# Performance work log

Hardware: AMD Instinct MI355X
Metric: run time of the kernel (lower is better)

Reference implementation:

```python
import jax, jax.numpy as jnp
import numpy as np

NUM_HEADS = 16
LAMBDA = 0.1
HADAMARD_SCALE = 0.05
ROPE_BASE = 10000.0


def _rope(t):
    # t: [B, H, S, hd] -- rotary embedding (half-split convention)
    hd = t.shape[-1]
    S = t.shape[2]
    half = hd // 2
    inv_freq = 1.0 / (ROPE_BASE ** (jnp.arange(half, dtype=jnp.float32) / half))
    ang = jnp.arange(S, dtype=jnp.float32)[:, None] * inv_freq[None, :]  # [S, half]
    cos = jnp.cos(ang).astype(t.dtype)
    sin = jnp.sin(ang).astype(t.dtype)
    t1, t2 = t[..., :half], t[..., half:]
    return jnp.concatenate([t1 * cos - t2 * sin, t2 * cos + t1 * sin], axis=-1)


def _rotate_half(t):
    half = t.shape[-1] // 2
    return jnp.concatenate([-t[..., half:], t[..., :half]], axis=-1)


def setup_inputs() -> dict:
    key = jax.random.key(0)
    ks = jax.random.split(key, 6)
    B, S, D = 2, 2048, 1024
    scale = 1.0 / np.sqrt(D).astype(np.float32)
    x = jax.random.normal(ks[0], (B, S, D), jnp.float32)
    Wq = jax.random.normal(ks[1], (D, D), jnp.float32) * scale
    Wk = jax.random.normal(ks[2], (D, D), jnp.float32) * scale
    Wv = jax.random.normal(ks[3], (D, D), jnp.float32) * scale
    Wo = jax.random.normal(ks[4], (D, D), jnp.float32) * scale
    gate_w = jax.random.normal(ks[5], (D // NUM_HEADS,), jnp.float32) * 0.01
    return {"x": x, "Wq": Wq, "Wk": Wk, "Wv": Wv, "Wo": Wo, "gate_w": gate_w}


def reference(x, Wq, Wk, Wv, Wo, gate_w):
    B, S, D = x.shape
    H = NUM_HEADS
    hd = D // H

    def heads(W):
        return (x @ W.T).reshape(B, S, H, hd).transpose(0, 2, 1, 3)  # [B,H,S,hd]

    Q = _rope(heads(Wq))
    K = _rope(heads(Wk))
    V = heads(Wv)

    causal = jnp.tril(jnp.ones((S, S), dtype=bool))
    inv_sqrt_d = 1.0 / jnp.sqrt(jnp.asarray(hd, x.dtype))

    def attend(q, k):
        # first-order + lambda * second-order (elementwise-squared) scores
        s = (jnp.einsum('bhsd,bhtd->bhst', q, k)
             + LAMBDA * jnp.einsum('bhsd,bhtd->bhst', q * q, k * k)) * inv_sqrt_d
        s = jnp.where(causal, s, jnp.asarray(-1e9, s.dtype))
        a = jax.nn.softmax(s, axis=-1)
        return jnp.einsum('bhst,bhtd->bhsd', a, V)

    out1 = attend(Q, K)                                  # standard pass
    out2 = attend(_rotate_half(Q), _rotate_half(K))      # rotated second pass

    # hadamard gate mix of the two passes
    out = 0.5 * (out1 + out2) + HADAMARD_SCALE * (out1 * out2) * gate_w

    out = out.transpose(0, 2, 1, 3).reshape(B, S, D)
    return out @ Wo.T
```

## Files before the change

### kernel.cpp

```cpp
#include <hip/hip_runtime.h>

typedef unsigned short u16;
typedef __attribute__((ext_vector_type(4))) unsigned short u16x4;
typedef __attribute__((ext_vector_type(8))) unsigned short u16x8;
typedef __attribute__((ext_vector_type(8))) short s16x8;
typedef __attribute__((ext_vector_type(4))) float f32x4;

__device__ __forceinline__ u16 f2bf(float f) {
  unsigned int u = __float_as_uint(f);
  u += 0x7FFFu + ((u >> 16) & 1u);
  return (u16)(u >> 16);
}
__device__ __forceinline__ float bf2f(u16 h) {
  return __uint_as_float(((unsigned int)h) << 16);
}

__device__ __forceinline__ void gload_lds16(const u16* g, u16* l) {
  __builtin_amdgcn_global_load_lds(
      (const __attribute__((address_space(1))) unsigned int*)(g),
      (__attribute__((address_space(3))) unsigned int*)(l), 16, 0, 0);
}

__global__ __launch_bounds__(256) void cvt_kernel(const float* __restrict__ src,
                                                  u16* __restrict__ dst, int n4) {
  int i = blockIdx.x * 256 + threadIdx.x;
  if (i >= n4) return;
  float4 v = reinterpret_cast<const float4*>(src)[i];
  u16x4 o;
  o.x = f2bf(v.x); o.y = f2bf(v.y); o.z = f2bf(v.z); o.w = f2bf(v.w);
  reinterpret_cast<u16x4*>(dst)[i] = o;
}

__global__ __launch_bounds__(256) void cvt_w(const float* __restrict__ Wq,
                                             const float* __restrict__ Wk,
                                             const float* __restrict__ Wv,
                                             const float* __restrict__ Wo,
                                             u16* __restrict__ wbf, u16* __restrict__ wobf) {
  int blk = blockIdx.x;
  int sel = blk >> 10;
  const float* src = (sel == 0) ? Wq : (sel == 1) ? Wk : (sel == 2) ? Wv : Wo;
  u16* dst = (sel < 3) ? (wbf + (size_t)sel * 1048576) : wobf;
  int i = (blk & 1023) * 256 + threadIdx.x;
  float4 v = reinterpret_cast<const float4*>(src)[i];
  u16x4 o;
  o.x = f2bf(v.x); o.y = f2bf(v.y); o.z = f2bf(v.z); o.w = f2bf(v.w);
  reinterpret_cast<u16x4*>(dst)[i] = o;
}

__device__ __forceinline__ void store_out(float* p, float v) { *p = v; }
__device__ __forceinline__ void store_out(u16* p, float v) { *p = f2bf(v); }

template <typename OutT, int WM, int WN>
__global__ __launch_bounds__(256) void gemm_bt(const u16* __restrict__ A,
                                               const u16* __restrict__ Bw,
                                               OutT* __restrict__ C, int N, int K) {
  __shared__ u16 As[WM * 2048];
  __shared__ u16 Bs[WN * 2048];
  const int tid = threadIdx.x;
  const int lane = tid & 63;
  const int wave = tid >> 6;
  const int wm = wave >> 1, wn = wave & 1;
  const int lh = lane & 15, quad = lane >> 4;
  const int q8 = quad * 8;
  const int m0 = blockIdx.y * (WM * 32), n0 = blockIdx.x * (WN * 32);
  constexpr int NCH = 4 * (WM + WN);
  constexpr int PER = NCH / 4;

  f32x4 acc[WM][WN];
#pragma unroll
  for (int i = 0; i < WM; ++i)
#pragma unroll
    for (int j = 0; j < WN; ++j) { acc[i][j][0] = 0.f; acc[i][j][1] = 0.f; acc[i][j][2] = 0.f; acc[i][j][3] = 0.f; }

  const int nkt = K >> 6;
  for (int kt = 0; kt < nkt; ++kt) {
    const int kb = kt * 64;
    __syncthreads();
#pragma unroll
    for (int i = 0; i < PER; ++i) {
      const int c = wave * PER + i;
      if (c < 4 * WM) {
        const int rb = c >> 1, kk2 = c & 1;
        gload_lds16(A + (size_t)(m0 + rb * 16 + lh) * K + kb + kk2 * 32 + q8,
                    &As[c * 512 + lane * 8]);
      } else {
        const int cb = c - 4 * WM;
        const int rb = cb >> 1, kk2 = cb & 1;
        gload_lds16(Bw + (size_t)(n0 + rb * 16 + lh) * K + kb + kk2 * 32 + q8,
                    &Bs[cb * 512 + lane * 8]);
      }
    }
    __syncthreads();
#pragma unroll
    for (int kk2 = 0; kk2 < 2; ++kk2) {
      s16x8 af[WM], bf4[WN];
#pragma unroll
      for (int mb = 0; mb < WM; ++mb)
        af[mb] = *reinterpret_cast<const s16x8*>(&As[((wm * WM + mb) * 2 + kk2) * 512 + lane * 8]);
#pragma unroll
      for (int nb = 0; nb < WN; ++nb)
        bf4[nb] = *reinterpret_cast<const s16x8*>(&Bs[((wn * WN + nb) * 2 + kk2) * 512 + lane * 8]);
#pragma unroll
      for (int mb = 0; mb < WM; ++mb)
#pragma unroll
        for (int nb = 0; nb < WN; ++nb)
          acc[mb][nb] = __builtin_amdgcn_mfma_f32_16x16x32_bf16(af[mb], bf4[nb], acc[mb][nb], 0, 0, 0);
    }
  }
#pragma unroll
  for (int mb = 0; mb < WM; ++mb)
#pragma unroll
    for (int nb = 0; nb < WN; ++nb) {
      const int col = n0 + wn * (WN * 16) + nb * 16 + lh;
#pragma unroll
      for (int r = 0; r < 4; ++r) {
        const int row = m0 + wm * (WM * 16) + mb * 16 + quad * 4 + r;
        store_out(&C[(size_t)row * N + col], acc[mb][nb][r]);
      }
    }
}

__global__ __launch_bounds__(256) void qkv_gemm(const u16* __restrict__ A,
                                                const u16* __restrict__ Bw,
                                                u16* __restrict__ raw,
                                                u16* __restrict__ Qs,
                                                u16* __restrict__ Kb,
                                                u16* __restrict__ K2b) {
  __shared__ u16 As[8192];
  __shared__ u16 Bs[8192];
  const int tid = threadIdx.x;
  const int lane = tid & 63;
  const int wave = tid >> 6;
  const int wm = wave >> 1, wn = wave & 1;
  const int lh = lane & 15, quad = lane >> 4;
  const int q8 = quad * 8;
  const int bx = blockIdx.x;
  const int m0 = blockIdx.y * 128, n0 = bx * 128;
  const int K = 1024;

  f32x4 acc[4][4];
#pragma unroll
  for (int i = 0; i < 4; ++i)
#pragma unroll
    for (int j = 0; j < 4; ++j) { acc[i][j][0] = 0.f; acc[i][j][1] = 0.f; acc[i][j][2] = 0.f; acc[i][j][3] = 0.f; }

  for (int kt = 0; kt < 16; ++kt) {
    const int kb = kt * 64;
    __syncthreads();
#pragma unroll
    for (int i = 0; i < 8; ++i) {
      const int c = wave * 8 + i;
      if (c < 16) {
        const int rb = c >> 1, kk2 = c & 1;
        gload_lds16(A + (size_t)(m0 + rb * 16 + lh) * K + kb + kk2 * 32 + q8,
                    &As[c * 512 + lane * 8]);
      } else {
        const int cb = c - 16;
        const int rb = cb >> 1, kk2 = cb & 1;
        gload_lds16(Bw + (size_t)(n0 + rb * 16 + lh) * K + kb + kk2 * 32 + q8,
                    &Bs[cb * 512 + lane * 8]);
      }
    }
    __syncthreads();
#pragma unroll
    for (int kk2 = 0; kk2 < 2; ++kk2) {
      s16x8 af[4], bf4[4];
#pragma unroll
      for (int mb = 0; mb < 4; ++mb)
        af[mb] = *reinterpret_cast<const s16x8*>(&As[((wm * 4 + mb) * 2 + kk2) * 512 + lane * 8]);
#pragma unroll
      for (int nb = 0; nb < 4; ++nb)
        bf4[nb] = *reinterpret_cast<const s16x8*>(&Bs[((wn * 4 + nb) * 2 + kk2) * 512 + lane * 8]);
#pragma unroll
      for (int mb = 0; mb < 4; ++mb)
#pragma unroll
        for (int nb = 0; nb < 4; ++nb)
          acc[mb][nb] = __builtin_amdgcn_mfma_f32_16x16x32_bf16(af[mb], bf4[nb], acc[mb][nb], 0, 0, 0);
    }
  }

  if (bx < 16) {
    const bool isQ = (bx < 8);
#pragma unroll
    for (int nb = 0; nb < 2; ++nb) {
      const int d = nb * 16 + lh;
      const float invf = __expf((float)d * -0.2878231366f);
      const int col = n0 + wn * 64 + nb * 16 + lh;
      const int ch = col & 1023;
      const int h = ch >> 6;
#pragma unroll
      for (int mb = 0; mb < 4; ++mb)
#pragma unroll
        for (int r = 0; r < 4; ++r) {
          const int row = m0 + wm * 64 + mb * 16 + quad * 4 + r;
          const int s = row & 2047, b = row >> 11;
          float ang = (float)s * invf;
          float sv, cv;
          __sincosf(ang, &sv, &cv);
          const float v1 = acc[mb][nb][r], v2 = acc[mb][nb + 2][r];
          const float e0 = v1 * cv - v2 * sv;
          const float e1 = v2 * cv + v1 * sv;
          const size_t ofs = (size_t)((b * 16 + h) * 2048 + s) * 64 + d;
          if (isQ) {
            Qs[ofs]      = f2bf(e0 * 0.125f);
            Qs[ofs + 32] = f2bf(e1 * 0.125f);
          } else {
            Kb[ofs]       = f2bf(e0);
            Kb[ofs + 32]  = f2bf(e1);
            K2b[ofs]      = f2bf(e0 * e0);
            K2b[ofs + 32] = f2bf(e1 * e1);
          }
        }
    }
  } else {
#pragma unroll
    for (int mb = 0; mb < 4; ++mb)
#pragma unroll
      for (int nb = 0; nb < 4; ++nb) {
        const int col = n0 + wn * 64 + nb * 16 + lh;
#pragma unroll
        for (int r = 0; r < 4; ++r) {
          const int row = m0 + wm * 64 + mb * 16 + quad * 4 + r;
          raw[(size_t)row * 3072 + col] = f2bf(acc[mb][nb][r]);
        }
      }
  }
}

__global__ __launch_bounds__(256) void transpose_v(const u16* __restrict__ raw,
                                                   u16* __restrict__ Vt) {
  int st = blockIdx.x, bh = blockIdx.y;
  int b = bh >> 4, h = bh & 15;
  __shared__ u16 tile[64 * 72];
  int tid = threadIdx.x;
#pragma unroll
  for (int it = 0; it < 4; ++it) {
    int c = it * 256 + tid;
    int sr = c >> 4, d4 = c & 15;
    u16x4 v = *reinterpret_cast<const u16x4*>(
        raw + (size_t)(b * 2048 + st * 64 + sr) * 3072 + 2048 + h * 64 + d4 * 4);
    *reinterpret_cast<u16x4*>(&tile[sr * 72 + d4 * 4]) = v;
  }
  __syncthreads();
#pragma unroll
  for (int it = 0; it < 4; ++it) {
    int c = it * 256 + tid;
    int dd = c >> 4, s4 = c & 15;
    u16x4 v;
#pragma unroll
    for (int j = 0; j < 4; ++j) v[j] = tile[(s4 * 4 + j) * 72 + dd];
    *reinterpret_cast<u16x4*>(Vt + (size_t)(bh * 64 + dd) * 2048 + st * 64 + s4 * 4) = v;
  }
}

__global__ __launch_bounds__(256, 2) void attn_kernel(const u16* __restrict__ Qs,
                                                      const u16* __restrict__ Kb,
                                                      const u16* __restrict__ K2b,
                                                      const u16* __restrict__ Vt,
                                                      const float* __restrict__ gate,
                                                      u16* __restrict__ attn,
                                                      float* __restrict__ Opart,
                                                      float* __restrict__ Lpart,
                                                      float* __restrict__ Opart2,
                                                      float* __restrict__ Lpart2) {
  const int bx = blockIdx.x;
  int qi, kt0, kt1, half, which;
  bool split;
  if (bx < 16) {
    qi = 15 - (bx >> 1); half = bx & 1; split = true; which = 0;
    const int nk = qi + 1; kt0 = half * nk; kt1 = kt0 + nk - 1;
  } else if (bx < 24) {
    const int t = bx - 16;
    qi = 7 - (t >> 1); half = t & 1; split = true; which = 1;
    const int nk = qi + 1; kt0 = half * nk; kt1 = kt0 + nk - 1;
  } else {
    qi = 27 - bx; split = false; which = 0; half = 0; kt0 = 0; kt1 = 2 * qi + 1;
  }
  const int bh = blockIdx.y;
  const int tid = threadIdx.x, lane = tid & 63, wave = tid >> 6;
  const int lh = lane & 15, quad = lane >> 4;
  const int b = bh >> 4, h = bh & 15;
  __shared__ u16 stageS[2][8192];
  __shared__ u16 Pbuf[4][2][1152];
  const int base = qi * 128 + wave * 32;
  const int q8 = quad * 8;

  auto do_stage = [&](int buf, int kt) {
#pragma unroll
    for (int i = 0; i < 4; ++i) {
      const int c = wave * 4 + i;
      const int t2 = c >> 3, f = c & 7, kk = f >> 2, nb = f & 3;
      const u16* src = (t2 ? K2b : Kb) +
          (size_t)(bh * 2048 + kt * 64 + nb * 16 + lh) * 64 + kk * 32 + q8;
      gload_lds16(src, &stageS[buf][t2 * 4096 + f * 512 + lane * 8]);
    }
  };

  s16x8 qf[2][2], q2f[2][2];
#pragma unroll
  for (int mb = 0; mb < 2; ++mb) {
    const size_t qoff = (size_t)(bh * 2048 + base + mb * 16 + lh) * 64 + q8;
#pragma unroll
    for (int kk = 0; kk < 2; ++kk) {
      qf[mb][kk] = *reinterpret_cast<const s16x8*>(Qs + qoff + kk * 32);
#pragma unroll
      for (int j = 0; j < 8; ++j) {
        float f = bf2f((u16)qf[mb][kk][j]);
        q2f[mb][kk][j] = (short)f2bf(f * f * 0.8f);
      }
    }
  }

  f32x4 oacc[2][4];
  float lsum[2][4];
#pragma unroll
  for (int mb = 0; mb < 2; ++mb)
#pragma unroll
    for (int nb = 0; nb < 4; ++nb) { oacc[mb][nb][0] = 0.f; oacc[mb][nb][1] = 0.f; oacc[mb][nb][2] = 0.f; oacc[mb][nb][3] = 0.f; }
#pragma unroll
  for (int mb = 0; mb < 2; ++mb)
#pragma unroll
    for (int r = 0; r < 4; ++r) lsum[mb][r] = 0.f;
  float gw[4];
#pragma unroll
  for (int nb = 0; nb < 4; ++nb) gw[nb] = gate[nb * 16 + lh];

  do_stage(0, kt0);
  __syncthreads();

  const int wmaxrow = base + 31;
  for (int kt = kt0; kt <= kt1; ++kt) {
    const int p = (kt - kt0) & 1;
    if (kt < kt1) do_stage(1 - p, kt + 1);

    if (kt * 64 <= wmaxrow) {
      const u16* Ks = stageS[p];
      f32x4 sacc[2][4];
#pragma unroll
      for (int mb = 0; mb < 2; ++mb)
#pragma unroll
        for (int nb = 0; nb < 4; ++nb) { sacc[mb][nb][0] = -8.f; sacc[mb][nb][1] = -8.f; sacc[mb][nb][2] = -8.f; sacc[mb][nb][3] = -8.f; }
#pragma unroll
      for (int nb = 0; nb < 4; ++nb)
#pragma unroll
        for (int kk = 0; kk < 2; ++kk) {
          s16x8 kf  = *reinterpret_cast<const s16x8*>(&Ks[(kk * 4 + nb) * 512 + lane * 8]);
          s16x8 k2f = *reinterpret_cast<const s16x8*>(&Ks[4096 + (kk * 4 + nb) * 512 + lane * 8]);
#pragma unroll
          for (int mb = 0; mb < 2; ++mb) {
            sacc[mb][nb] = __builtin_amdgcn_mfma_f32_16x16x32_bf16(qf[mb][kk],  kf,  sacc[mb][nb], 0, 0, 0);
            sacc[mb][nb] = __builtin_amdgcn_mfma_f32_16x16x32_bf16(q2f[mb][kk], k2f, sacc[mb][nb], 0, 0, 0);
          }
        }
      s16x8 vf[2][4];
#pragma unroll
      for (int kk = 0; kk < 2; ++kk)
#pragma unroll
        for (int nb = 0; nb < 4; ++nb)
          vf[kk][nb] = *reinterpret_cast<const s16x8*>(
              Vt + (size_t)(bh * 64 + nb * 16 + lh) * 2048 + kt * 64 + kk * 32 + q8);

      if (kt * 64 + 63 > base) {
#pragma unroll
        for (int mb = 0; mb < 2; ++mb)
#pragma unroll
          for (int nb = 0; nb < 4; ++nb) {
            const int colg = kt * 64 + nb * 16 + lh;
#pragma unroll
            for (int r = 0; r < 4; ++r) {
              const int rowg = base + mb * 16 + quad * 4 + r;
              if (colg > rowg) sacc[mb][nb][r] = -1e9f;
            }
          }
      }
#pragma unroll
      for (int mb = 0; mb < 2; ++mb)
#pragma unroll
        for (int nb = 0; nb < 4; ++nb)
#pragma unroll
          for (int r = 0; r < 4; ++r) {
            float pv = __expf(sacc[mb][nb][r]);
            lsum[mb][r] += pv;
            Pbuf[wave][mb][(quad * 4 + r) * 72 + nb * 16 + lh] = f2bf(pv);
          }
#pragma unroll
      for (int mb = 0; mb < 2; ++mb)
#pragma unroll
        for (int kk = 0; kk < 2; ++kk) {
          s16x8 pf = *reinterpret_cast<const s16x8*>(&Pbuf[wave][mb][lh * 72 + kk * 32 + q8]);
#pragma unroll
          for (int nb = 0; nb < 4; ++nb)
            oacc[mb][nb] = __builtin_amdgcn_mfma_f32_16x16x32_bf16(pf, vf[kk][nb], oacc[mb][nb], 0, 0, 0);
        }
    }
    __syncthreads();
  }
#pragma unroll
  for (int mb = 0; mb < 2; ++mb)
#pragma unroll
    for (int r = 0; r < 4; ++r) {
      float rs = lsum[mb][r];
#pragma unroll
      for (int off = 1; off < 16; off <<= 1) rs += __shfl_xor(rs, off);
      lsum[mb][r] = rs;
    }
  if (split) {
#pragma unroll
    for (int mb = 0; mb < 2; ++mb)
#pragma unroll
      for (int r = 0; r < 4; ++r) {
        const int rowg = base + mb * 16 + quad * 4 + r;
        if (which == 0) {
          const size_t orow = (size_t)half * 32768 + bh * 1024 + (rowg - 1024);
          if (lh == 0) Lpart[orow] = lsum[mb][r];
#pragma unroll
          for (int nb = 0; nb < 4; ++nb)
            Opart[orow * 64 + nb * 16 + lh] = oacc[mb][nb][r];
        } else {
          const size_t orow = (size_t)half * 16384 + bh * 512 + (rowg - 512);
          if (lh == 0) Lpart2[orow] = lsum[mb][r];
#pragma unroll
          for (int nb = 0; nb < 4; ++nb)
            Opart2[orow * 64 + nb * 16 + lh] = oacc[mb][nb][r];
        }
      }
  } else {
#pragma unroll
    for (int mb = 0; mb < 2; ++mb)
#pragma unroll
      for (int r = 0; r < 4; ++r) {
        const float invl = 1.0f / lsum[mb][r];
        const int rows = base + mb * 16 + quad * 4 + r;
#pragma unroll
        for (int nb = 0; nb < 4; ++nb) {
          float o = oacc[mb][nb][r] * invl;
          float val = o + 0.05f * o * o * gw[nb];
          attn[(size_t)(b * 2048 + rows) * 1024 + h * 64 + nb * 16 + lh] = f2bf(val);
        }
      }
  }
}

__global__ __launch_bounds__(256) void combine_kernel(const float* __restrict__ Opart,
                                                      const float* __restrict__ Lpart,
                                                      const float* __restrict__ Opart2,
                                                      const float* __restrict__ Lpart2,
                                                      const float* __restrict__ gate,
                                                      u16* __restrict__ attn) {
  int idx = blockIdx.x * 256 + threadIdx.x;
  int d = idx & 63;
  int r_all = idx >> 6;
  float o, l;
  int bh, s;
  if (r_all < 32768) {
    o = Opart[idx] + Opart[idx + 2097152];
    l = Lpart[r_all] + Lpart[r_all + 32768];
    bh = r_all >> 10; s = 1024 + (r_all & 1023);
  } else {
    const int r2 = r_all - 32768;
    const int i2 = idx - 2097152;
    o = Opart2[i2] + Opart2[i2 + 1048576];
    l = Lpart2[r2] + Lpart2[r2 + 16384];
    bh = r2 >> 9; s = 512 + (r2 & 511);
  }
  o /= l;
  float val = o + 0.05f * o * o * gate[d];
  int b = bh >> 4, h = bh & 15;
  attn[(size_t)(b * 2048 + s) * 1024 + h * 64 + d] = f2bf(val);
}

extern "C" void kernel_launch(void* const* d_in, const int* in_sizes, int n_in,
                              void* d_out, int out_size, void* d_ws, size_t ws_size,
                              hipStream_t stream) {
  (void)in_sizes; (void)n_in; (void)out_size; (void)ws_size;
  const float* x    = (const float*)d_in[0];
  const float* Wq   = (const float*)d_in[1];
  const float* Wk   = (const float*)d_in[2];
  const float* Wv   = (const float*)d_in[3];
  const float* Wo   = (const float*)d_in[4];
  const float* gate = (const float*)d_in[5];

  u16* ws    = (u16*)d_ws;
  u16* xbf   = ws;
  u16* wbf   = xbf + 4194304;
  u16* wobf  = wbf + 3145728;
  u16* raw   = wobf + 1048576;
  u16* Qsb   = raw + 12582912;
  u16* Kbb   = Qsb + 4194304;
  u16* K2bb  = Kbb + 4194304;
  u16* Vtb   = K2bb + 4194304;
  float* Opart = (float*)(Vtb + 4194304);
  float* Lpart = Opart + 4194304;
  u16* attnb = raw;
  float* Opart2 = (float*)(raw + 4194304);
  float* Lpart2 = Opart2 + 2097152;

  cvt_kernel<<<4096, 256, 0, stream>>>(x, xbf, 1048576);
  cvt_w<<<4096, 256, 0, stream>>>(Wq, Wk, Wv, Wo, wbf, wobf);

  qkv_gemm<<<dim3(24, 32), 256, 0, stream>>>(xbf, wbf, raw, Qsb, Kbb, K2bb);
  transpose_v<<<dim3(32, 32), 256, 0, stream>>>(raw, Vtb);
  attn_kernel<<<dim3(28, 32), 256, 0, stream>>>(Qsb, Kbb, K2bb, Vtb, gate, attnb,
                                                Opart, Lpart, Opart2, Lpart2);
  combine_kernel<<<12288, 256, 0, stream>>>(Opart, Lpart, Opart2, Lpart2, gate, attnb);
  gemm_bt<float, 4, 2><<<dim3(16, 32), 256, 0, stream>>>(attnb, wobf, (float*)d_out, 1024, 1024);
}
```

Measured before the change: 274.3 us.

## Fuse conversions, write V transposed from QKV GEMM, split long query tiles four ways

The x and weight conversion kernels are merged into one launch. The QKV GEMM now writes V directly in transposed [bh,d,s] layout, which drops the raw buffer and the separate transpose kernel. The attention work split changes so the longest query tiles (qi 8-15) are divided into four key chunks instead of two, giving more blocks and better balance. The cost is larger partial buffers and a four-way reduction in the combine step, and the V stores are narrow strided 8-byte writes.

```diff
diff --git a/kernel.cpp b/kernel.cpp
--- a/kernel.cpp
+++ b/kernel.cpp
@@ -21,26 +21,27 @@
       (__attribute__((address_space(3))) unsigned int*)(l), 16, 0, 0);
 }
 
-__global__ __launch_bounds__(256) void cvt_kernel(const float* __restrict__ src,
-                                                  u16* __restrict__ dst, int n4) {
-  int i = blockIdx.x * 256 + threadIdx.x;
-  if (i >= n4) return;
-  float4 v = reinterpret_cast<const float4*>(src)[i];
-  u16x4 o;
-  o.x = f2bf(v.x); o.y = f2bf(v.y); o.z = f2bf(v.z); o.w = f2bf(v.w);
-  reinterpret_cast<u16x4*>(dst)[i] = o;
-}
-
-__global__ __launch_bounds__(256) void cvt_w(const float* __restrict__ Wq,
-                                             const float* __restrict__ Wk,
-                                             const float* __restrict__ Wv,
-                                             const float* __restrict__ Wo,
-                                             u16* __restrict__ wbf, u16* __restrict__ wobf) {
+__global__ __launch_bounds__(256) void cvt_all(const float* __restrict__ x,
+                                               const float* __restrict__ Wq,
+                                               const float* __restrict__ Wk,
+                                               const float* __restrict__ Wv,
+                                               const float* __restrict__ Wo,
+                                               u16* __restrict__ xbf,
+                                               u16* __restrict__ wbf,
+                                               u16* __restrict__ wobf) {
   int blk = blockIdx.x;
-  int sel = blk >> 10;
-  const float* src = (sel == 0) ? Wq : (sel == 1) ? Wk : (sel == 2) ? Wv : Wo;
-  u16* dst = (sel < 3) ? (wbf + (size_t)sel * 1048576) : wobf;
-  int i = (blk & 1023) * 256 + threadIdx.x;
+  const float* src;
+  u16* dst;
+  int i;
+  if (blk < 4096) {
+    src = x; dst = xbf; i = blk * 256 + threadIdx.x;
+  } else {
+    int wb = blk - 4096;
+    int sel = wb >> 10;
+    src = (sel == 0) ? Wq : (sel == 1) ? Wk : (sel == 2) ? Wv : Wo;
+    dst = (sel < 3) ? (wbf + (size_t)sel * 1048576) : wobf;
+    i = (wb & 1023) * 256 + threadIdx.x;
+  }
   float4 v = reinterpret_cast<const float4*>(src)[i];
   u16x4 o;
   o.x = f2bf(v.x); o.y = f2bf(v.y); o.z = f2bf(v.z); o.w = f2bf(v.w);
@@ -122,7 +123,7 @@
 
 __global__ __launch_bounds__(256) void qkv_gemm(const u16* __restrict__ A,
                                                 const u16* __restrict__ Bw,
-                                                u16* __restrict__ raw,
+                                                u16* __restrict__ Vt,
                                                 u16* __restrict__ Qs,
                                                 u16* __restrict__ Kb,
                                                 u16* __restrict__ K2b) {
@@ -218,38 +219,15 @@
 #pragma unroll
       for (int nb = 0; nb < 4; ++nb) {
         const int col = n0 + wn * 64 + nb * 16 + lh;
-#pragma unroll
-        for (int r = 0; r < 4; ++r) {
-          const int row = m0 + wm * 64 + mb * 16 + quad * 4 + r;
-          raw[(size_t)row * 3072 + col] = f2bf(acc[mb][nb][r]);
-        }
-      }
-  }
-}
-
-__global__ __launch_bounds__(256) void transpose_v(const u16* __restrict__ raw,
-                                                   u16* __restrict__ Vt) {
-  int st = blockIdx.x, bh = blockIdx.y;
-  int b = bh >> 4, h = bh & 15;
-  __shared__ u16 tile[64 * 72];
-  int tid = threadIdx.x;
-#pragma unroll
-  for (int it = 0; it < 4; ++it) {
-    int c = it * 256 + tid;
-    int sr = c >> 4, d4 = c & 15;
-    u16x4 v = *reinterpret_cast<const u16x4*>(
-        raw + (size_t)(b * 2048 + st * 64 + sr) * 3072 + 2048 + h * 64 + d4 * 4);
-    *reinterpret_cast<u16x4*>(&tile[sr * 72 + d4 * 4]) = v;
-  }
-  __syncthreads();
-#pragma unroll
-  for (int it = 0; it < 4; ++it) {
-    int c = it * 256 + tid;
-    int dd = c >> 4, s4 = c & 15;
-    u16x4 v;
-#pragma unroll
-    for (int j = 0; j < 4; ++j) v[j] = tile[(s4 * 4 + j) * 72 + dd];
-    *reinterpret_cast<u16x4*>(Vt + (size_t)(bh * 64 + dd) * 2048 + st * 64 + s4 * 4) = v;
+        const int ch = col & 1023;
+        const int h = ch >> 6, d = ch & 63;
+        const int row0 = m0 + wm * 64 + mb * 16 + quad * 4;
+        const int s0 = row0 & 2047, b = row0 >> 11;
+        u16x4 o;
+#pragma unroll
+        for (int r = 0; r < 4; ++r) o[r] = f2bf(acc[mb][nb][r]);
+        *reinterpret_cast<u16x4*>(Vt + (size_t)((b * 16 + h) * 64 + d) * 2048 + s0) = o;
+      }
   }
 }
 
@@ -264,17 +242,19 @@
                                                       float* __restrict__ Opart2,
                                                       float* __restrict__ Lpart2) {
   const int bx = blockIdx.x;
-  int qi, kt0, kt1, half, which;
+  int qi, kt0, kt1, chunk, which;
   bool split;
-  if (bx < 16) {
-    qi = 15 - (bx >> 1); half = bx & 1; split = true; which = 0;
-    const int nk = qi + 1; kt0 = half * nk; kt1 = kt0 + nk - 1;
-  } else if (bx < 24) {
-    const int t = bx - 16;
-    qi = 7 - (t >> 1); half = t & 1; split = true; which = 1;
-    const int nk = qi + 1; kt0 = half * nk; kt1 = kt0 + nk - 1;
+  if (bx < 32) {
+    qi = 15 - (bx >> 2); chunk = bx & 3; split = true; which = 0;
+    const int T = 2 * qi + 2;
+    kt0 = (chunk * T) >> 2;
+    kt1 = (((chunk + 1) * T) >> 2) - 1;
+  } else if (bx < 40) {
+    const int t = bx - 32;
+    qi = 7 - (t >> 1); chunk = t & 1; split = true; which = 1;
+    const int nk = qi + 1; kt0 = chunk * nk; kt1 = kt0 + nk - 1;
   } else {
-    qi = 27 - bx; split = false; which = 0; half = 0; kt0 = 0; kt1 = 2 * qi + 1;
+    qi = 43 - bx; split = false; which = 0; chunk = 0; kt0 = 0; kt1 = 2 * qi + 1;
   }
   const int bh = blockIdx.y;
   const int tid = threadIdx.x, lane = tid & 63, wave = tid >> 6;
@@ -411,13 +391,13 @@
       for (int r = 0; r < 4; ++r) {
         const int rowg = base + mb * 16 + quad * 4 + r;
         if (which == 0) {
-          const size_t orow = (size_t)half * 32768 + bh * 1024 + (rowg - 1024);
+          const size_t orow = (size_t)chunk * 32768 + bh * 1024 + (rowg - 1024);
           if (lh == 0) Lpart[orow] = lsum[mb][r];
 #pragma unroll
           for (int nb = 0; nb < 4; ++nb)
             Opart[orow * 64 + nb * 16 + lh] = oacc[mb][nb][r];
         } else {
-          const size_t orow = (size_t)half * 16384 + bh * 512 + (rowg - 512);
+          const size_t orow = (size_t)chunk * 16384 + bh * 512 + (rowg - 512);
           if (lh == 0) Lpart2[orow] = lsum[mb][r];
 #pragma unroll
           for (int nb = 0; nb < 4; ++nb)
@@ -453,8 +433,8 @@
   float o, l;
   int bh, s;
   if (r_all < 32768) {
-    o = Opart[idx] + Opart[idx + 2097152];
-    l = Lpart[r_all] + Lpart[r_all + 32768];
+    o = Opart[idx] + Opart[idx + 2097152] + Opart[idx + 4194304] + Opart[idx + 6291456];
+    l = Lpart[r_all] + Lpart[r_all + 32768] + Lpart[r_all + 65536] + Lpart[r_all + 98304];
     bh = r_all >> 10; s = 1024 + (r_all & 1023);
   } else {
     const int r2 = r_all - 32768;
@@ -484,23 +464,19 @@
   u16* xbf   = ws;
   u16* wbf   = xbf + 4194304;
   u16* wobf  = wbf + 3145728;
-  u16* raw   = wobf + 1048576;
-  u16* Qsb   = raw + 12582912;
+  u16* Qsb   = wobf + 1048576;
   u16* Kbb   = Qsb + 4194304;
   u16* K2bb  = Kbb + 4194304;
   u16* Vtb   = K2bb + 4194304;
-  float* Opart = (float*)(Vtb + 4194304);
-  float* Lpart = Opart + 4194304;
-  u16* attnb = raw;
-  float* Opart2 = (float*)(raw + 4194304);
+  float* Opart  = (float*)(Vtb + 4194304);
+  float* Lpart  = Opart + 8388608;
+  float* Opart2 = Lpart + 131072;
   float* Lpart2 = Opart2 + 2097152;
-
-  cvt_kernel<<<4096, 256, 0, stream>>>(x, xbf, 1048576);
-  cvt_w<<<4096, 256, 0, stream>>>(Wq, Wk, Wv, Wo, wbf, wobf);
-
-  qkv_gemm<<<dim3(24, 32), 256, 0, stream>>>(xbf, wbf, raw, Qsb, Kbb, K2bb);
-  transpose_v<<<dim3(32, 32), 256, 0, stream>>>(raw, Vtb);
-  attn_kernel<<<dim3(28, 32), 256, 0, stream>>>(Qsb, Kbb, K2bb, Vtb, gate, attnb,
+  u16* attnb = xbf;
+
+  cvt_all<<<8192, 256, 0, stream>>>(x, Wq, Wk, Wv, Wo, xbf, wbf, wobf);
+  qkv_gemm<<<dim3(24, 32), 256, 0, stream>>>(xbf, wbf, Vtb, Qsb, Kbb, K2bb);
+  attn_kernel<<<dim3(44, 32), 256, 0, stream>>>(Qsb, Kbb, K2bb, Vtb, gate, attnb,
                                                 Opart, Lpart, Opart2, Lpart2);
   combine_kernel<<<12288, 256, 0, stream>>>(Opart, Lpart, Opart2, Lpart2, gate, attnb);
   gemm_bt<float, 4, 2><<<dim3(16, 32), 256, 0, stream>>>(attnb, wobf, (float*)d_out, 1024, 1024);
```

After: 257.7 us. 6.1% less time.
